# Optimization experiments

Measured on AMD Instinct MI355X. Metric: run time of the kernel, lower is better.

Reference implementation:

```python
import jax, jax.numpy as jnp
import numpy as np

# BM25 constants (canonical values; N/Lave ~ MS MARCO passage corpus)
K1 = 1.2
K3 = 8.0
B = 0.75
N_DOCS = 8841823.0
LAVE = 56.0
VOCAB = 1_000_000
L = 8_388_608  # tokens per side (query / passage)


def setup_inputs() -> dict:
    key = jax.random.key(0)
    k_ids, k_df = jax.random.split(key, 2)
    ids = jax.random.randint(k_ids, (2, L), 0, VOCAB, dtype=jnp.int32)
    masks = jnp.ones((2, L), dtype=jnp.int32)  # unused by the original forward
    # document-frequency table, positive counts well below N_DOCS
    DF = jax.random.uniform(k_df, (VOCAB,), dtype=jnp.float32) * 10000.0 + 1.0
    return {"ids": ids, "masks": masks, "DF": DF}


def reference(ids, masks, DF):
    q = ids[0]          # [L] query token ids
    p = ids[1]          # [L] passage token ids
    vocab = DF.shape[0]
    Ld = jnp.float32(p.shape[0])

    # fused histogram (term-frequency) counting: one scatter-add pass per side
    hq = jnp.zeros((vocab,), jnp.float32).at[q].add(1.0)
    hp = jnp.zeros((vocab,), jnp.float32).at[p].add(1.0)

    # per-query-token gathers (matches the per-id equality+sum of the loop)
    qtf = hq[q]         # [L] count of q[i] within the query
    ptf = hp[q]         # [L] count of q[i] within the passage
    df = DF[q]          # [L] document frequency lookup

    idf = jnp.log2((N_DOCS - df + 0.5) / (df + 0.5))
    denom = ptf + K1 * (1.0 - B + B * Ld / LAVE)
    term = (qtf / (K3 + qtf)) * (K1 * ptf / denom) * idf
    score = jnp.sum(term)
    return jax.nn.sigmoid(score)
```

## Files before the change

### kernel.cpp

```cpp
#include <hip/hip_runtime.h>
#include <math.h>

typedef unsigned int u32;
typedef unsigned short u16;

#define SHIFT 11
#define SBINS 2048
#define NBMAX 512
#define CAPS 48
#define TILE_I4 4096
#define TILE_IDS (TILE_I4 * 4)
#define SC_TPB 512
#define HS_TPB 512
#define RD_TPB 256

__global__ __launch_bounds__(SC_TPB) void
scatter_kernel(const int4* __restrict__ ids4, u32* __restrict__ seg,
               float* __restrict__ acc, int nb) {
    __shared__ u32 staged32[NBMAX * (CAPS / 2)];
    __shared__ u32 lcur[NBMAX];
    int tid = threadIdx.x;
    int t = blockIdx.x;
    if (t == 0 && tid == 0) *acc = 0.0f;
    int nw = nb * (CAPS / 2);
    for (int j = tid; j < nw; j += SC_TPB) staged32[j] = 0xFFFFFFFFu;
    for (int k = tid; k < nb; k += SC_TPB) lcur[k] = (u32)k * CAPS;
    __syncthreads();

    u16* staged = (u16*)staged32;
    int base = t * TILE_I4;
    u32 w[32];
#pragma unroll
    for (int j = 0; j < 8; ++j) {
        int4 v = ids4[base + tid + j * SC_TPB];
        w[4 * j + 0] = (u32)v.x; w[4 * j + 1] = (u32)v.y;
        w[4 * j + 2] = (u32)v.z; w[4 * j + 3] = (u32)v.w;
    }
#pragma unroll
    for (int e = 0; e < 32; ++e) {
        u32 id = w[e];
        u32 k = id >> SHIFT;
        u32 pos = atomicAdd(&lcur[k], 1u);
        if (pos < (k + 1u) * CAPS)
            staged[pos] = (u16)(id & (SBINS - 1));
    }
    __syncthreads();
    uint4* __restrict__ dst = (uint4*)(seg + (size_t)t * nw);
    const uint4* __restrict__ src = (const uint4*)staged32;
    int nv4 = nw >> 2;
    for (int j = tid; j < nv4; j += SC_TPB) dst[j] = src[j];
}

__global__ __launch_bounds__(HS_TPB) void
hist_side_kernel(const uint2* __restrict__ seg2, u32* __restrict__ ghist,
                 int nb, int NT) {
    __shared__ u32 h[SBINS];
    int bi = blockIdx.x;
    int s = (bi >= nb) ? 1 : 0;
    int b = bi - s * nb;
    int tid = threadIdx.x;
    for (int k = tid; k < SBINS; k += HS_TPB) h[k] = 0u;
    __syncthreads();

    const u32 C2 = CAPS / 4;
    u32 pt2 = (u32)nb * C2;
    size_t sbase = (size_t)s * NT * pt2 + (u32)b * C2;
    int n2 = NT * (int)C2;
    for (int j = tid; j < n2; j += HS_TPB) {
        u32 ts = (u32)j / C2;
        u32 ww = (u32)j - ts * C2;
        uint2 x = seg2[sbase + (size_t)ts * pt2 + ww];
        u32 a0 = x.x & 0xFFFFu, a1 = x.x >> 16;
        u32 a2 = x.y & 0xFFFFu, a3 = x.y >> 16;
        if (a0 < SBINS) atomicAdd(&h[a0], 1u);
        if (a1 < SBINS) atomicAdd(&h[a1], 1u);
        if (a2 < SBINS) atomicAdd(&h[a2], 1u);
        if (a3 < SBINS) atomicAdd(&h[a3], 1u);
    }
    __syncthreads();
    u32* __restrict__ dstp = ghist + (size_t)s * nb * SBINS + (size_t)b * SBINS;
    for (int k = tid; k < SBINS; k += HS_TPB) dstp[k] = h[k];
}

__global__ __launch_bounds__(RD_TPB) void
reduce_kernel(const u32* __restrict__ gq, const u32* __restrict__ gp,
              const float* __restrict__ DF, float* __restrict__ acc,
              int nbins, int vocab, float denom_c) {
    int i = blockIdx.x * RD_TPB + threadIdx.x;
    int stride = gridDim.x * RD_TPB;
    float sum = 0.0f;
    for (; i < nbins; i += stride) {
        u32 q = gq[i];
        if (i < vocab && q) {
            float qtf = (float)q;
            float ptf = (float)gp[i];
            float dfv = DF[i];
            float idf = log2f((8841823.0f - dfv + 0.5f) / (dfv + 0.5f));
            sum += qtf * (qtf / (8.0f + qtf)) * (1.2f * ptf / (ptf + denom_c)) * idf;
        }
    }
#pragma unroll
    for (int o = 32; o > 0; o >>= 1) sum += __shfl_down(sum, o, 64);
    __shared__ float ls[RD_TPB / 64];
    int wid = threadIdx.x >> 6;
    if ((threadIdx.x & 63) == 0) ls[wid] = sum;
    __syncthreads();
    if (threadIdx.x == 0) {
        float ssum = 0.0f;
        for (int wv = 0; wv < RD_TPB / 64; ++wv) ssum += ls[wv];
        atomicAdd(acc, ssum);
    }
}

__global__ void final_kernel(const float* __restrict__ acc, float* __restrict__ out) {
    float s = *acc;
    out[0] = 1.0f / (1.0f + expf(-s));
}


__global__ void zero_ws_kernel(uint4* __restrict__ ws, int n4) {
    int i = blockIdx.x * blockDim.x + threadIdx.x;
    int stride = gridDim.x * blockDim.x;
    uint4 z = make_uint4(0u, 0u, 0u, 0u);
    for (; i < n4; i += stride) ws[i] = z;
}

__global__ void hist_kernel(const int4* __restrict__ ids4, unsigned* __restrict__ hq,
                            unsigned* __restrict__ hp, int L4) {
    int i = blockIdx.x * blockDim.x + threadIdx.x;
    int stride = gridDim.x * blockDim.x;
    int n4 = 2 * L4;
    for (; i < n4; i += stride) {
        int4 t = ids4[i];
        unsigned* __restrict__ h = (i < L4) ? hq : hp;
        atomicAdd(&h[t.x], 1u); atomicAdd(&h[t.y], 1u);
        atomicAdd(&h[t.z], 1u); atomicAdd(&h[t.w], 1u);
    }
}

__global__ void score_kernel_slow(const int4* __restrict__ q4, const unsigned* __restrict__ hq,
                                  const unsigned* __restrict__ hp, const float* __restrict__ DF,
                                  float* __restrict__ acc, int L4, float denom_c) {
    int i = blockIdx.x * blockDim.x + threadIdx.x;
    int stride = gridDim.x * blockDim.x;
    float sum = 0.0f;
    for (; i < L4; i += stride) {
        int4 t = q4[i];
        int id[4] = {t.x, t.y, t.z, t.w};
#pragma unroll
        for (int k = 0; k < 4; ++k) {
            float qtf = (float)hq[id[k]];
            float ptf = (float)hp[id[k]];
            float dfv = DF[id[k]];
            float idf = log2f((8841823.0f - dfv + 0.5f) / (dfv + 0.5f));
            sum += (qtf / (8.0f + qtf)) * (1.2f * ptf / (ptf + denom_c)) * idf;
        }
    }
    for (int o = 32; o > 0; o >>= 1) sum += __shfl_down(sum, o, 64);
    __shared__ float ls[8];
    int wid = threadIdx.x >> 6;
    if ((threadIdx.x & 63) == 0) ls[wid] = sum;
    __syncthreads();
    if (threadIdx.x == 0) {
        float s = 0.0f;
        int nw = blockDim.x >> 6;
        for (int w = 0; w < nw; ++w) s += ls[w];
        atomicAdd(acc, s);
    }
}


extern "C" void kernel_launch(void* const* d_in, const int* in_sizes, int n_in,
                              void* d_out, int out_size, void* d_ws, size_t ws_size,
                              hipStream_t stream) {
    const int* ids = (const int*)d_in[0];
    const float* DF = (const float*)d_in[2];
    float* out = (float*)d_out;

    int n_ids = in_sizes[0];
    int L = n_ids / 2;
    int vocab = in_sizes[2];
    int nb = (vocab + SBINS - 1) >> SHIFT;
    float denom_c = (float)(1.2 * (1.0 - 0.75 + 0.75 * (double)L / 56.0));

    int NT = L / TILE_IDS;
    double mpt = (double)TILE_IDS / (double)nb;
    size_t seg_bytes = (size_t)2 * NT * nb * CAPS * 2;
    size_t ghist_bytes = (size_t)2 * nb * SBINS * 4;
    size_t need = seg_bytes + ghist_bytes + 64;
    bool fast = (ws_size >= need) && (n_ids % 8 == 0) && (L % TILE_IDS == 0) &&
                (nb <= NBMAX) && (mpt + 2.0 * sqrt(mpt) <= (double)CAPS);

    if (fast) {
        u32* seg = (u32*)d_ws;
        u32* ghist = (u32*)((char*)d_ws + seg_bytes);
        float* acc = (float*)((char*)d_ws + seg_bytes + ghist_bytes);
        int nbins = nb * SBINS;

        scatter_kernel<<<2 * NT, SC_TPB, 0, stream>>>((const int4*)ids, seg, acc, nb);
        hist_side_kernel<<<2 * nb, HS_TPB, 0, stream>>>((const uint2*)seg, ghist, nb, NT);
        reduce_kernel<<<512, RD_TPB, 0, stream>>>(ghist, ghist + nbins, DF, acc,
                                                  nbins, vocab, denom_c);
        final_kernel<<<1, 1, 0, stream>>>(acc, out);
    } else {
        unsigned* hq = (unsigned*)d_ws;
        unsigned* hp = hq + vocab;
        float* acc = (float*)(hp + vocab);
        int L4 = L / 4;
        int zwords = 2 * vocab + 4;
        zero_ws_kernel<<<1024, 256, 0, stream>>>((uint4*)d_ws, zwords / 4);
        hist_kernel<<<2048, 256, 0, stream>>>((const int4*)ids, hq, hp, L4);
        score_kernel_slow<<<2048, 256, 0, stream>>>((const int4*)ids, hq, hp, DF, acc, L4, denom_c);
        final_kernel<<<1, 1, 0, stream>>>(acc, out);
    }
}
```

Measured before the change: 169.1 us.

## Fuse final sigmoid into reduce via ticket, widen scatter and hist loads

Folds the single-thread sigmoid kernel into the reduce kernel with a last-block ticket counter, which removes one launch. The scatter kernel now runs 1024 threads per block and issues all its LDS atomics before doing the staged stores, which exposes more memory-level parallelism. The histogram kernel reads 16-byte vectors instead of 8-byte ones, and the reduce grid grows to 1024 blocks. The cost is higher register pressure in the scatter kernel and one extra global atomic per reduce block.

```diff
diff --git a/kernel.cpp b/kernel.cpp
--- a/kernel.cpp
+++ b/kernel.cpp
@@ -10,18 +10,19 @@
 #define CAPS 48
 #define TILE_I4 4096
 #define TILE_IDS (TILE_I4 * 4)
-#define SC_TPB 512
+#define SC_TPB 1024
+#define IPT4 (TILE_I4 / SC_TPB)
 #define HS_TPB 512
 #define RD_TPB 256
 
 __global__ __launch_bounds__(SC_TPB) void
 scatter_kernel(const int4* __restrict__ ids4, u32* __restrict__ seg,
-               float* __restrict__ acc, int nb) {
+               float* __restrict__ acc, u32* __restrict__ ticket, int nb) {
     __shared__ u32 staged32[NBMAX * (CAPS / 2)];
     __shared__ u32 lcur[NBMAX];
     int tid = threadIdx.x;
     int t = blockIdx.x;
-    if (t == 0 && tid == 0) *acc = 0.0f;
+    if (t == 0 && tid == 0) { *acc = 0.0f; *ticket = 0u; }
     int nw = nb * (CAPS / 2);
     for (int j = tid; j < nw; j += SC_TPB) staged32[j] = 0xFFFFFFFFu;
     for (int k = tid; k < nb; k += SC_TPB) lcur[k] = (u32)k * CAPS;
@@ -29,20 +30,22 @@
 
     u16* staged = (u16*)staged32;
     int base = t * TILE_I4;
-    u32 w[32];
-#pragma unroll
-    for (int j = 0; j < 8; ++j) {
+    u32 w[IPT4 * 4];
+#pragma unroll
+    for (int j = 0; j < IPT4; ++j) {
         int4 v = ids4[base + tid + j * SC_TPB];
         w[4 * j + 0] = (u32)v.x; w[4 * j + 1] = (u32)v.y;
         w[4 * j + 2] = (u32)v.z; w[4 * j + 3] = (u32)v.w;
     }
-#pragma unroll
-    for (int e = 0; e < 32; ++e) {
-        u32 id = w[e];
-        u32 k = id >> SHIFT;
-        u32 pos = atomicAdd(&lcur[k], 1u);
-        if (pos < (k + 1u) * CAPS)
-            staged[pos] = (u16)(id & (SBINS - 1));
+    u32 pos[IPT4 * 4];
+#pragma unroll
+    for (int e = 0; e < IPT4 * 4; ++e)
+        pos[e] = atomicAdd(&lcur[w[e] >> SHIFT], 1u);
+#pragma unroll
+    for (int e = 0; e < IPT4 * 4; ++e) {
+        u32 k = w[e] >> SHIFT;
+        if (pos[e] < (k + 1u) * CAPS)
+            staged[pos[e]] = (u16)(w[e] & (SBINS - 1));
     }
     __syncthreads();
     uint4* __restrict__ dst = (uint4*)(seg + (size_t)t * nw);
@@ -52,7 +55,7 @@
 }
 
 __global__ __launch_bounds__(HS_TPB) void
-hist_side_kernel(const uint2* __restrict__ seg2, u32* __restrict__ ghist,
+hist_side_kernel(const uint4* __restrict__ seg4, u32* __restrict__ ghist,
                  int nb, int NT) {
     __shared__ u32 h[SBINS];
     int bi = blockIdx.x;
@@ -62,20 +65,23 @@
     for (int k = tid; k < SBINS; k += HS_TPB) h[k] = 0u;
     __syncthreads();
 
-    const u32 C2 = CAPS / 4;
-    u32 pt2 = (u32)nb * C2;
-    size_t sbase = (size_t)s * NT * pt2 + (u32)b * C2;
-    int n2 = NT * (int)C2;
-    for (int j = tid; j < n2; j += HS_TPB) {
-        u32 ts = (u32)j / C2;
-        u32 ww = (u32)j - ts * C2;
-        uint2 x = seg2[sbase + (size_t)ts * pt2 + ww];
-        u32 a0 = x.x & 0xFFFFu, a1 = x.x >> 16;
-        u32 a2 = x.y & 0xFFFFu, a3 = x.y >> 16;
-        if (a0 < SBINS) atomicAdd(&h[a0], 1u);
-        if (a1 < SBINS) atomicAdd(&h[a1], 1u);
-        if (a2 < SBINS) atomicAdd(&h[a2], 1u);
-        if (a3 < SBINS) atomicAdd(&h[a3], 1u);
+    const u32 C4 = CAPS / 8;
+    u32 pt4 = (u32)nb * C4;
+    size_t sbase = (size_t)s * NT * pt4 + (u32)b * C4;
+    int n4 = NT * (int)C4;
+    for (int j = tid; j < n4; j += HS_TPB) {
+        u32 ts = (u32)j / C4;
+        u32 ww = (u32)j - ts * C4;
+        uint4 x = seg4[sbase + (size_t)ts * pt4 + ww];
+        u32 a;
+        a = x.x & 0xFFFFu; if (a < SBINS) atomicAdd(&h[a], 1u);
+        a = x.x >> 16;     if (a < SBINS) atomicAdd(&h[a], 1u);
+        a = x.y & 0xFFFFu; if (a < SBINS) atomicAdd(&h[a], 1u);
+        a = x.y >> 16;     if (a < SBINS) atomicAdd(&h[a], 1u);
+        a = x.z & 0xFFFFu; if (a < SBINS) atomicAdd(&h[a], 1u);
+        a = x.z >> 16;     if (a < SBINS) atomicAdd(&h[a], 1u);
+        a = x.w & 0xFFFFu; if (a < SBINS) atomicAdd(&h[a], 1u);
+        a = x.w >> 16;     if (a < SBINS) atomicAdd(&h[a], 1u);
     }
     __syncthreads();
     u32* __restrict__ dstp = ghist + (size_t)s * nb * SBINS + (size_t)b * SBINS;
@@ -85,6 +91,7 @@
 __global__ __launch_bounds__(RD_TPB) void
 reduce_kernel(const u32* __restrict__ gq, const u32* __restrict__ gp,
               const float* __restrict__ DF, float* __restrict__ acc,
+              u32* __restrict__ ticket, float* __restrict__ out,
               int nbins, int vocab, float denom_c) {
     int i = blockIdx.x * RD_TPB + threadIdx.x;
     int stride = gridDim.x * RD_TPB;
@@ -109,12 +116,13 @@
         float ssum = 0.0f;
         for (int wv = 0; wv < RD_TPB / 64; ++wv) ssum += ls[wv];
         atomicAdd(acc, ssum);
-    }
-}
-
-__global__ void final_kernel(const float* __restrict__ acc, float* __restrict__ out) {
-    float s = *acc;
-    out[0] = 1.0f / (1.0f + expf(-s));
+        __threadfence();
+        u32 done = atomicAdd(ticket, 1u);
+        if (done == gridDim.x - 1u) {
+            float s = atomicAdd(acc, 0.0f);
+            out[0] = 1.0f / (1.0f + expf(-s));
+        }
+    }
 }
 
 
@@ -169,6 +177,11 @@
     }
 }
 
+__global__ void final_kernel(const float* __restrict__ acc, float* __restrict__ out) {
+    float s = *acc;
+    out[0] = 1.0f / (1.0f + expf(-s));
+}
+
 
 extern "C" void kernel_launch(void* const* d_in, const int* in_sizes, int n_in,
                               void* d_out, int out_size, void* d_ws, size_t ws_size,
@@ -195,13 +208,14 @@
         u32* seg = (u32*)d_ws;
         u32* ghist = (u32*)((char*)d_ws + seg_bytes);
         float* acc = (float*)((char*)d_ws + seg_bytes + ghist_bytes);
+        u32* ticket = (u32*)(acc + 1);
         int nbins = nb * SBINS;
-
-        scatter_kernel<<<2 * NT, SC_TPB, 0, stream>>>((const int4*)ids, seg, acc, nb);
-        hist_side_kernel<<<2 * nb, HS_TPB, 0, stream>>>((const uint2*)seg, ghist, nb, NT);
-        reduce_kernel<<<512, RD_TPB, 0, stream>>>(ghist, ghist + nbins, DF, acc,
-                                                  nbins, vocab, denom_c);
-        final_kernel<<<1, 1, 0, stream>>>(acc, out);
+        const int rd_blocks = 1024;
+
+        scatter_kernel<<<2 * NT, SC_TPB, 0, stream>>>((const int4*)ids, seg, acc, ticket, nb);
+        hist_side_kernel<<<2 * nb, HS_TPB, 0, stream>>>((const uint4*)seg, ghist, nb, NT);
+        reduce_kernel<<<rd_blocks, RD_TPB, 0, stream>>>(ghist, ghist + nbins, DF, acc,
+                                                        ticket, out, nbins, vocab, denom_c);
     } else {
         unsigned* hq = (unsigned*)d_ws;
         unsigned* hp = hq + vocab;
```

Result: slower. 187.8 us (+11.0%).
